# Optimization experiments

Hardware: AMD Instinct MI355X
Metric: run time of the kernel (lower is better)

## Reference

```python
import jax, jax.numpy as jnp
import numpy as np

V = 200000  # num entities
R = 100     # num relations
D = 128     # embedding_dim
K = 20      # entity_neighbor_num
B = 128     # batch (docs)
N = 50      # entities per doc


def setup_inputs() -> dict:
    key = jax.random.key(0)
    ks = jax.random.split(key, 8)
    return {
        "entity_ids": jax.random.randint(ks[0], (B, N), 0, V),
        "adj_entity": jax.random.randint(ks[1], (V, K), 0, V),
        "adj_relation": jax.random.randint(ks[2], (V, K), 0, R),
        "entity_embedding": jax.random.normal(ks[3], (V, D), jnp.float32),
        "relation_embedding": jax.random.normal(ks[4], (R, D), jnp.float32),
        "W_att": jax.random.normal(ks[5], (3 * D, 1), jnp.float32) * 0.05,
        "b_att": jnp.zeros((1,), jnp.float32),
        "W_conv": jax.random.normal(ks[6], (2 * D, D), jnp.float32) * 0.05,
        "b_conv": jnp.zeros((D,), jnp.float32),
    }


def reference(entity_ids, adj_entity, adj_relation, entity_embedding,
              relation_embedding, W_att, b_att, W_conv, b_conv):
    # neighbor ids: [B, N, K]
    neigh_ent = adj_entity[entity_ids]
    neigh_rel = adj_relation[entity_ids]
    ne = entity_embedding[neigh_ent]      # [B, N, K, D]
    nr = relation_embedding[neigh_rel]    # [B, N, K, D]
    ee = entity_embedding[entity_ids]     # [B, N, D]
    ee_exp = jnp.broadcast_to(ee[:, :, None, :], ne.shape)  # [B, N, K, D]
    concat = jnp.concatenate([ee_exp, ne, nr], axis=-1)     # [B, N, K, 3D]
    logits = jax.nn.relu(concat @ W_att + b_att)            # [B, N, K, 1]
    # NOTE: faithful to original nn.Softmax(dim=0) -> softmax over batch axis
    att = jax.nn.softmax(logits, axis=0)                    # [B, N, K, 1]
    neighbor_att = jnp.sum(att * ne, axis=2)                # [B, N, D]
    agg_in = jnp.concatenate([ee, neighbor_att], axis=-1)   # [B, N, 2D]
    return jax.nn.relu(agg_in @ W_conv + b_conv)            # [B, N, D]
```

## Files before the change

### kernel.cpp

```cpp
#include <hip/hip_runtime.h>

#define V 200000
#define R 100
#define D 128
#define K 20
#define B 128
#define N 50

__global__ void k_logits(const int* __restrict__ eids,
                         const int* __restrict__ adjE,
                         const int* __restrict__ adjR,
                         const float* __restrict__ EE,
                         const float* __restrict__ RE,
                         const float* __restrict__ Watt,
                         const float* __restrict__ batt,
                         float* __restrict__ att) {
  const int lane = threadIdx.x & 63;
  const int wv   = threadIdx.x >> 6;
  const int bn   = blockIdx.x * 4 + wv;
  const int b = bn / N;
  const int n = bn % N;
  const int eid = eids[bn];

  const float2 wa_e = ((const float2*)Watt)[lane];
  const float2 e2   = ((const float2*)(EE + (size_t)eid * D))[lane];
  float p = e2.x * wa_e.x + e2.y * wa_e.y;
  #pragma unroll
  for (int off = 32; off > 0; off >>= 1) p += __shfl_down(p, off);
  const float s_ee = __shfl(p, 0) + batt[0];

  const int g  = lane >> 4;
  const int sl = lane & 15;
  const float4* wnp = (const float4*)(Watt + D + 8 * sl);
  const float4* wrp = (const float4*)(Watt + 2 * D + 8 * sl);
  const float4 wn0 = wnp[0], wn1 = wnp[1];
  const float4 wr0 = wrp[0], wr1 = wrp[1];

  const int* ae = adjE + eid * K;
  const int* ar = adjR + eid * K;

  float q[5];
  #pragma unroll
  for (int k5 = 0; k5 < 5; ++k5) {
    const int k = k5 * 4 + g;
    const int nid = ae[k];
    const int rid = ar[k];
    const float4* np = (const float4*)(EE + (size_t)nid * D + 8 * sl);
    const float4* rp = (const float4*)(RE + (size_t)rid * D + 8 * sl);
    const float4 n0 = np[0], n1 = np[1];
    const float4 r0 = rp[0], r1 = rp[1];
    float s = n0.x * wn0.x + n0.y * wn0.y + n0.z * wn0.z + n0.w * wn0.w
            + n1.x * wn1.x + n1.y * wn1.y + n1.z * wn1.z + n1.w * wn1.w
            + r0.x * wr0.x + r0.y * wr0.y + r0.z * wr0.z + r0.w * wr0.w
            + r1.x * wr1.x + r1.y * wr1.y + r1.z * wr1.z + r1.w * wr1.w;
    #pragma unroll
    for (int off = 8; off > 0; off >>= 1) s += __shfl_down(s, off, 16);
    q[k5] = s;
  }

  if (sl == 0) {
    #pragma unroll
    for (int k5 = 0; k5 < 5; ++k5) {
      const int k = k5 * 4 + g;
      const float logit = s_ee + q[k5];
      att[(n * K + k) * B + b] = logit > 0.0f ? logit : 0.0f;
    }
  }
}

__global__ void k_softmax(float* __restrict__ att) {
  __shared__ float red[4];
  const int gg = blockIdx.x;
  const int t = threadIdx.x;
  const float x = att[gg * B + t];

  float m = x;
  #pragma unroll
  for (int off = 32; off > 0; off >>= 1) m = fmaxf(m, __shfl_down(m, off));
  if ((t & 63) == 0) red[t >> 6] = m;
  __syncthreads();
  const float mm = fmaxf(red[0], red[1]);

  const float e = __expf(x - mm);
  float s = e;
  #pragma unroll
  for (int off = 32; off > 0; off >>= 1) s += __shfl_down(s, off);
  if ((t & 63) == 0) red[2 + (t >> 6)] = s;
  __syncthreads();
  const float ss = red[2] + red[3];

  att[gg * B + t] = e / ss;
}

#define G 8
__global__ void k_out(const int* __restrict__ eids,
                      const int* __restrict__ adjE,
                      const float* __restrict__ EE,
                      const float* __restrict__ att,
                      const float* __restrict__ Wc,
                      const float* __restrict__ bc,
                      float* __restrict__ out) {
  __shared__ float agg[G][2 * D];
  __shared__ float part[4][G][D];
  __shared__ float s_att[G][K];
  __shared__ int   s_nid[G][K];

  const int t = threadIdx.x;
  const int d = t & 127;
  const int h = t >> 7;
  const int base = blockIdx.x * G;

  if (t < G * K) {
    const int j = t / K, k = t % K;
    const int bn = base + j;
    const int b = bn / N;
    const int n = bn % N;
    const int eid = eids[bn];
    s_nid[j][k] = adjE[eid * K + k];
    s_att[j][k] = att[(n * K + k) * B + b];
  }
  __syncthreads();

  #pragma unroll
  for (int jj = 0; jj < G / 2; ++jj) {
    const int j = h + jj * 2;
    const int bn = base + j;
    const int eid = eids[bn];
    const float ee = EE[(size_t)eid * D + d];
    float na = 0.0f;
    #pragma unroll
    for (int k = 0; k < K; ++k)
      na += s_att[j][k] * EE[(size_t)s_nid[j][k] * D + d];
    agg[j][d] = ee;
    agg[j][D + d] = na;
  }
  __syncthreads();

  {
    const int d2 = t & 63;
    const int h4 = t >> 6;
    float accx[G], accy[G];
    #pragma unroll
    for (int j = 0; j < G; ++j) { accx[j] = 0.0f; accy[j] = 0.0f; }
    const int ibase = h4 * 64;
    for (int c = 0; c < 16; ++c) {
      const int i = ibase + c * 4;
      const float2 w0 = *(const float2*)&Wc[(i + 0) * D + 2 * d2];
      const float2 w1 = *(const float2*)&Wc[(i + 1) * D + 2 * d2];
      const float2 w2 = *(const float2*)&Wc[(i + 2) * D + 2 * d2];
      const float2 w3 = *(const float2*)&Wc[(i + 3) * D + 2 * d2];
      #pragma unroll
      for (int j = 0; j < G; ++j) {
        const float4 a = *(const float4*)&agg[j][i];
        accx[j] += a.x * w0.x + a.y * w1.x + a.z * w2.x + a.w * w3.x;
        accy[j] += a.x * w0.y + a.y * w1.y + a.z * w2.y + a.w * w3.y;
      }
    }
    #pragma unroll
    for (int j = 0; j < G; ++j)
      *(float2*)&part[h4][j][2 * d2] = make_float2(accx[j], accy[j]);
  }
  __syncthreads();

  const float bb = bc[d];
  #pragma unroll
  for (int jj = 0; jj < 4; ++jj) {
    const int j = h * 4 + jj;
    const float v = part[0][j][d] + part[1][j][d] + part[2][j][d]
                  + part[3][j][d] + bb;
    out[(size_t)(base + j) * D + d] = v > 0.0f ? v : 0.0f;
  }
}

extern "C" void kernel_launch(void* const* d_in, const int* in_sizes, int n_in,
                              void* d_out, int out_size, void* d_ws, size_t ws_size,
                              hipStream_t stream) {
  const int*   eids = (const int*)d_in[0];
  const int*   adjE = (const int*)d_in[1];
  const int*   adjR = (const int*)d_in[2];
  const float* EE   = (const float*)d_in[3];
  const float* RE   = (const float*)d_in[4];
  const float* Watt = (const float*)d_in[5];
  const float* batt = (const float*)d_in[6];
  const float* Wc   = (const float*)d_in[7];
  const float* bc   = (const float*)d_in[8];
  float* out = (float*)d_out;

  float* att = (float*)d_ws;

  k_logits<<<(B * N) / 4, 256, 0, stream>>>(eids, adjE, adjR, EE, RE, Watt,
                                            batt, att);
  k_softmax<<<N * K, 128, 0, stream>>>(att);
  k_out<<<(B * N) / G, 256, 0, stream>>>(eids, adjE, EE, att, Wc, bc, out);
}
```

Before: 202.8 us.

## Fuse softmax into logits via atomic denominators and halve k_out group size

The separate softmax kernel is removed. The logits kernel now writes exp(relu(logit)) and atomically adds it into a per-(n,k) denominator, which is zeroed by a small new kernel, and k_out divides by that denominator when loading attention weights. Max subtraction is dropped, which relies on the logits staying small enough not to overflow exp. The group size in k_out is halved to 4, doubling block count at the cost of less reuse of W_conv.

```diff
diff --git a/kernel.cpp b/kernel.cpp
--- a/kernel.cpp
+++ b/kernel.cpp
@@ -7,6 +7,11 @@
 #define B 128
 #define N 50
 
+__global__ void k_zero(float* __restrict__ denom) {
+  const int i = blockIdx.x * 256 + threadIdx.x;
+  if (i < N * K) denom[i] = 0.0f;
+}
+
 __global__ void k_logits(const int* __restrict__ eids,
                          const int* __restrict__ adjE,
                          const int* __restrict__ adjR,
@@ -14,7 +19,8 @@
                          const float* __restrict__ RE,
                          const float* __restrict__ Watt,
                          const float* __restrict__ batt,
-                         float* __restrict__ att) {
+                         float* __restrict__ att,
+                         float* __restrict__ denom) {
   const int lane = threadIdx.x & 63;
   const int wv   = threadIdx.x >> 6;
   const int bn   = blockIdx.x * 4 + wv;
@@ -63,40 +69,20 @@
     for (int k5 = 0; k5 < 5; ++k5) {
       const int k = k5 * 4 + g;
       const float logit = s_ee + q[k5];
-      att[(n * K + k) * B + b] = logit > 0.0f ? logit : 0.0f;
+      const float rl = logit > 0.0f ? logit : 0.0f;
+      const float e = __expf(rl);
+      att[(n * K + k) * B + b] = e;
+      atomicAdd(&denom[n * K + k], e);
     }
   }
 }
 
-__global__ void k_softmax(float* __restrict__ att) {
-  __shared__ float red[4];
-  const int gg = blockIdx.x;
-  const int t = threadIdx.x;
-  const float x = att[gg * B + t];
-
-  float m = x;
-  #pragma unroll
-  for (int off = 32; off > 0; off >>= 1) m = fmaxf(m, __shfl_down(m, off));
-  if ((t & 63) == 0) red[t >> 6] = m;
-  __syncthreads();
-  const float mm = fmaxf(red[0], red[1]);
-
-  const float e = __expf(x - mm);
-  float s = e;
-  #pragma unroll
-  for (int off = 32; off > 0; off >>= 1) s += __shfl_down(s, off);
-  if ((t & 63) == 0) red[2 + (t >> 6)] = s;
-  __syncthreads();
-  const float ss = red[2] + red[3];
-
-  att[gg * B + t] = e / ss;
-}
-
-#define G 8
+#define G 4
 __global__ void k_out(const int* __restrict__ eids,
                       const int* __restrict__ adjE,
                       const float* __restrict__ EE,
                       const float* __restrict__ att,
+                      const float* __restrict__ denom,
                       const float* __restrict__ Wc,
                       const float* __restrict__ bc,
                       float* __restrict__ out) {
@@ -117,7 +103,7 @@
     const int n = bn % N;
     const int eid = eids[bn];
     s_nid[j][k] = adjE[eid * K + k];
-    s_att[j][k] = att[(n * K + k) * B + b];
+    s_att[j][k] = att[(n * K + k) * B + b] / denom[n * K + k];
   }
   __syncthreads();
 
@@ -164,8 +150,8 @@
 
   const float bb = bc[d];
   #pragma unroll
-  for (int jj = 0; jj < 4; ++jj) {
-    const int j = h * 4 + jj;
+  for (int jj = 0; jj < G / 2; ++jj) {
+    const int j = h * 2 + jj;
     const float v = part[0][j][d] + part[1][j][d] + part[2][j][d]
                   + part[3][j][d] + bb;
     out[(size_t)(base + j) * D + d] = v > 0.0f ? v : 0.0f;
@@ -186,10 +172,12 @@
   const float* bc   = (const float*)d_in[8];
   float* out = (float*)d_out;
 
-  float* att = (float*)d_ws;
+  float* att   = (float*)d_ws;
+  float* denom = att + (size_t)N * K * B;
 
+  k_zero<<<(N * K + 255) / 256, 256, 0, stream>>>(denom);
   k_logits<<<(B * N) / 4, 256, 0, stream>>>(eids, adjE, adjR, EE, RE, Watt,
-                                            batt, att);
-  k_softmax<<<N * K, 128, 0, stream>>>(att);
-  k_out<<<(B * N) / G, 256, 0, stream>>>(eids, adjE, EE, att, Wc, bc, out);
+                                            batt, att, denom);
+  k_out<<<(B * N) / G, 256, 0, stream>>>(eids, adjE, EE, att, denom, Wc, bc,
+                                         out);
 }
```

After: 210.6 us. 1.04x slower.
